# Kernel optimization log

Measured on AMD Instinct MI355X. Metric: run time of the kernel, lower is better.

Reference implementation:

```python
import jax, jax.numpy as jnp
import numpy as np
import math

B, T, C, H, L, V = 4, 2048, 256, 4, 2, 1024
HS = C // H  # head size


def setup_inputs() -> dict:
    key = jax.random.key(0)
    ks = jax.random.split(key, 10)
    s = 0.02
    return {
        "tokens": jax.random.randint(ks[0], (B, T), 0, V),
        "wte": s * jax.random.normal(ks[1], (V + 1, C), dtype=jnp.float32),
        "ln1_g": jnp.ones((L, C), jnp.float32),
        "ln1_b": jnp.zeros((L, C), jnp.float32),
        "attn_w": s * jax.random.normal(ks[2], (L, 3 * C, C), dtype=jnp.float32),
        "attn_b": jnp.zeros((L, 3 * C), jnp.float32),
        "proj_w": s * jax.random.normal(ks[3], (L, C, C), dtype=jnp.float32),
        "proj_b": jnp.zeros((L, C), jnp.float32),
        "embk": s * jax.random.normal(ks[4], (L, T, HS), dtype=jnp.float32),
        "embv": s * jax.random.normal(ks[5], (L, T, HS), dtype=jnp.float32),
        "ln2_g": jnp.ones((L, C), jnp.float32),
        "ln2_b": jnp.zeros((L, C), jnp.float32),
        "fc_w": s * jax.random.normal(ks[6], (L, 4 * C, C), dtype=jnp.float32),
        "fc_b": jnp.zeros((L, 4 * C), jnp.float32),
        "mproj_w": s * jax.random.normal(ks[7], (L, C, 4 * C), dtype=jnp.float32),
        "mproj_b": jnp.zeros((L, C), jnp.float32),
        "lnf_g": jnp.ones((C,), jnp.float32),
        "lnf_b": jnp.zeros((C,), jnp.float32),
        "head_w": s * jax.random.normal(ks[8], (V, C), dtype=jnp.float32),
    }


def _ln(x, g, b):
    mu = x.mean(-1, keepdims=True)
    var = x.var(-1, keepdims=True)
    return (x - mu) / jnp.sqrt(var + 1e-5) * g + b


def _gelu(x):  # NewGELU (tanh approximation)
    return 0.5 * x * (1.0 + jnp.tanh(math.sqrt(2.0 / math.pi) * (x + 0.044715 * x ** 3)))


def reference(tokens, wte, ln1_g, ln1_b, attn_w, attn_b, proj_w, proj_b,
              embk, embv, ln2_g, ln2_b, fc_w, fc_b, mproj_w, mproj_b,
              lnf_g, lnf_b, head_w):
    x = wte[tokens]  # [B,T,C]; no absolute pos emb in this model
    idx = jnp.arange(T)
    rel = jnp.tril(idx[:, None] - idx[None, :])  # [T,T] nonneg offsets
    causal = idx[:, None] >= idx[None, :]
    scale = 1.0 / math.sqrt(HS)
    for l in range(L):
        h = _ln(x, ln1_g[l], ln1_b[l])
        qkv = h @ attn_w[l].T + attn_b[l]  # [B,T,3C]
        q, k, v = jnp.split(qkv, 3, axis=-1)
        q = q.reshape(B, T, H, HS).transpose(0, 2, 1, 3)  # [B,H,T,hs]
        k = k.reshape(B, T, H, HS).transpose(0, 2, 1, 3)
        v = v.reshape(B, T, H, HS).transpose(0, 2, 1, 3)
        rk = embk[l][rel]  # [T,T,hs]
        rv = embv[l][rel]  # [T,T,hs]
        att = jnp.einsum('bhtd,bhsd->bhts', q, k) * scale \
            + jnp.einsum('bhtd,tsd->bhts', q, rk)
        att = jnp.where(causal, att, -jnp.inf)
        att = jax.nn.softmax(att, axis=-1)
        y = jnp.einsum('bhts,bhsd->bhtd', att, v) \
            + jnp.einsum('bhts,tsd->bhtd', att, rv)
        y = y.transpose(0, 2, 1, 3).reshape(B, T, C)
        x = x + (y @ proj_w[l].T + proj_b[l])
        h2 = _ln(x, ln2_g[l], ln2_b[l])
        x = x + (_gelu(h2 @ fc_w[l].T + fc_b[l]) @ mproj_w[l].T + mproj_b[l])
    x = _ln(x, lnf_g, lnf_b)
    return x @ head_w.T  # [B,T,V] logits
```

## Files before the change

### kernel.cpp

```cpp
#include <hip/hip_runtime.h>
#include <hip/hip_bf16.h>
#include <math.h>

#define BB 4
#define TT 2048
#define CC 256
#define HH 4
#define LL 2
#define VV 1024
#define HS 64
#define EPAD 2176
#define LOG2E 1.4426950408889634f

typedef __attribute__((ext_vector_type(8))) __bf16 bf16x8;
typedef __attribute__((ext_vector_type(4))) float f32x4;

#define MFMA16(a, b, c) __builtin_amdgcn_mfma_f32_16x16x32_bf16((a), (b), (c), 0, 0, 0)

__device__ __forceinline__ ushort f2bf(float f) {
    __hip_bfloat16 h = __float2bfloat16(f);
    return *reinterpret_cast<ushort*>(&h);
}
__device__ __forceinline__ float bf2f(ushort u) {
    union { uint i; float f; } c; c.i = ((uint)u) << 16; return c.f;
}

__device__ __forceinline__ void gload16(const void* g, void* l) {
    __builtin_amdgcn_global_load_lds(
        (const __attribute__((address_space(1))) void*)g,
        (__attribute__((address_space(3))) void*)l, 16, 0, 0);
}

__device__ __forceinline__ float gelu_f(float v) {
    return 0.5f * v * (1.0f + tanhf(0.7978845608028654f * (v + 0.044715f * v * v * v)));
}

__global__ void embed_kernel(const int* __restrict__ tok,
                             const float* __restrict__ wte,
                             float* __restrict__ x) {
    int row = blockIdx.x;
    int tid = threadIdx.x;
    int tk = tok[row];
    x[(size_t)row * CC + tid] = wte[(size_t)tk * CC + tid];
}

__global__ void cvt5_kernel(const float* __restrict__ w0, const float* __restrict__ w1,
                            const float* __restrict__ w2, const float* __restrict__ w3,
                            const float* __restrict__ w4,
                            ushort* __restrict__ o0, ushort* __restrict__ o1,
                            ushort* __restrict__ o2, ushort* __restrict__ o3,
                            ushort* __restrict__ o4) {
    int i = blockIdx.x * 256 + threadIdx.x;
    const float* src; ushort* dst; int j;
    if (i < 98304)       { src = w0; dst = o0; j = i; }
    else if (i < 131072) { src = w1; dst = o1; j = i - 98304; }
    else if (i < 262144) { src = w2; dst = o2; j = i - 131072; }
    else if (i < 393216) { src = w3; dst = o3; j = i - 262144; }
    else                 { src = w4; dst = o4; j = i - 393216; }
    float4 v = ((const float4*)src)[j];
    ushort4 o;
    o.x = f2bf(v.x); o.y = f2bf(v.y); o.z = f2bf(v.z); o.w = f2bf(v.w);
    ((ushort4*)dst)[j] = o;
}

__global__ __launch_bounds__(256) void ln_kernel(const float* __restrict__ x,
                                                 const float* __restrict__ g,
                                                 const float* __restrict__ b,
                                                 ushort* __restrict__ out) {
    int row = blockIdx.x * 4 + (threadIdx.x >> 6);
    int lane = threadIdx.x & 63;
    float4 v = ((const float4*)(x + (size_t)row * CC))[lane];
    float s = v.x + v.y + v.z + v.w;
    float s2 = v.x * v.x + v.y * v.y + v.z * v.z + v.w * v.w;
    for (int m = 1; m < 64; m <<= 1) {
        s += __shfl_xor(s, m);
        s2 += __shfl_xor(s2, m);
    }
    float mean = s * (1.0f / CC);
    float var = s2 * (1.0f / CC) - mean * mean;
    float rs = rsqrtf(var + 1e-5f);
    float4 gg = ((const float4*)g)[lane];
    float4 bb = ((const float4*)b)[lane];
    ushort4 o;
    o.x = f2bf((v.x - mean) * rs * gg.x + bb.x);
    o.y = f2bf((v.y - mean) * rs * gg.y + bb.y);
    o.z = f2bf((v.z - mean) * rs * gg.z + bb.z);
    o.w = f2bf((v.w - mean) * rs * gg.w + bb.w);
    ((ushort4*)(out + (size_t)row * CC))[lane] = o;
}

template<int MODE>
__global__ __launch_bounds__(256) void bgemm128_kernel(
        const ushort* __restrict__ A, const ushort* __restrict__ W,
        const float* __restrict__ bias, float* __restrict__ out,
        ushort* __restrict__ outb, int N, int K,
        ushort* __restrict__ qb, ushort* __restrict__ kb,
        ushort* __restrict__ vtb) {
    constexpr int ASUB = 8, TOT = 12, BUFSH = 192 * 32;
    __shared__ ushort lds[2 * BUFSH];
    int tid = threadIdx.x;
    int w = tid >> 6, lane = tid & 63;
    int lo = lane & 15, hi = lane >> 4;
    int row0 = blockIdx.y * 128;
    int col0 = blockIdx.x * 64;
    int wm = w >> 1, wn = w & 1;
    const ushort* Asrc = A + (size_t)row0 * K;
    const ushort* Wsrc = W + (size_t)col0 * K;

    auto STAGE = [&](int buf, int k0) {
        ushort* dst = &lds[buf * BUFSH];
        for (int s = w; s < TOT; s += 4) {
            const ushort* src;
            if (s < ASUB) src = Asrc + (size_t)(s * 16 + lo) * K + k0 + hi * 8;
            else          src = Wsrc + (size_t)((s - ASUB) * 16 + lo) * K + k0 + hi * 8;
            gload16(src, dst + s * 512);
        }
    };

    f32x4 acc[4][2] = {};
    int NT = K >> 5;
    STAGE(0, 0);
    asm volatile("s_waitcnt vmcnt(0)" ::: "memory");
    __syncthreads();
    for (int t = 0; t < NT; ++t) {
        int buf = t & 1;
        if (t + 1 < NT) STAGE(buf ^ 1, (t + 1) << 5);
        bf16x8 a[4], b[2];
#pragma unroll
        for (int f = 0; f < 4; ++f)
            a[f] = *(const bf16x8*)&lds[buf * BUFSH + (wm * 4 + f) * 512 + lane * 8];
#pragma unroll
        for (int g = 0; g < 2; ++g)
            b[g] = *(const bf16x8*)&lds[buf * BUFSH + (ASUB + wn * 2 + g) * 512 + lane * 8];
        __builtin_amdgcn_s_setprio(1);
#pragma unroll
        for (int f = 0; f < 4; ++f)
#pragma unroll
            for (int g = 0; g < 2; ++g)
                acc[f][g] = MFMA16(a[f], b[g], acc[f][g]);
        __builtin_amdgcn_s_setprio(0);
        asm volatile("s_waitcnt vmcnt(0)" ::: "memory");
        __syncthreads();
    }
#pragma unroll
    for (int f = 0; f < 4; ++f) {
        int rr = row0 + wm * 64 + f * 16 + hi * 4;
#pragma unroll
        for (int g = 0; g < 2; ++g) {
            int cc = col0 + wn * 32 + g * 16 + lo;
            float bv = bias ? bias[cc] : 0.0f;
#pragma unroll
            for (int j = 0; j < 4; ++j) {
                int r = rr + j;
                float v = acc[f][g][j] + bv;
                if (MODE == 3) {
                    int t = r & 2047, bb2 = r >> 11;
                    int which = cc >> 8, hh = (cc >> 6) & 3, dd = cc & 63;
                    size_t bh = (size_t)(bb2 * 4 + hh);
                    if (which == 0)      qb[(bh * 2048 + t) * 64 + dd] = f2bf(v);
                    else if (which == 1) kb[(bh * 2048 + t) * 64 + dd] = f2bf(v * (0.125f * LOG2E));
                    else                 vtb[(bh * 64 + dd) * 2048 + t] = f2bf(v);
                } else if (MODE == 2) {
                    outb[(size_t)r * N + cc] = f2bf(gelu_f(v));
                } else {
                    out[(size_t)r * N + cc] = v;
                }
            }
        }
    }
}

__global__ __launch_bounds__(256) void bgemm64_kernel(
        const ushort* __restrict__ A, const ushort* __restrict__ W,
        const float* __restrict__ bias, float* __restrict__ out,
        int N, int K) {
    constexpr int ASUB = 8, TOT = 16, BUFSH = 128 * 64;
    __shared__ ushort lds[2 * BUFSH];
    int tid = threadIdx.x;
    int w = tid >> 6, lane = tid & 63;
    int lo = lane & 15, hi = lane >> 4;
    int row0 = blockIdx.y * 64;
    int col0 = blockIdx.x * 64;
    const ushort* Asrc = A + (size_t)row0 * K;
    const ushort* Wsrc = W + (size_t)col0 * K;

    auto STAGE = [&](int buf, int k0) {
        ushort* dst = &lds[buf * BUFSH];
        for (int s = w; s < TOT; s += 4) {
            const ushort* src;
            if (s < ASUB) {
                int rg = s >> 1, kh = s & 1;
                src = Asrc + (size_t)(rg * 16 + lo) * K + k0 + kh * 32 + hi * 8;
            } else {
                int s2 = s - ASUB;
                int cg = s2 >> 1, kh = s2 & 1;
                src = Wsrc + (size_t)(cg * 16 + lo) * K + k0 + kh * 32 + hi * 8;
            }
            gload16(src, dst + s * 512);
        }
    };

    f32x4 acc[4] = {};
    int NT = K >> 6;
    STAGE(0, 0);
    asm volatile("s_waitcnt vmcnt(0)" ::: "memory");
    __syncthreads();
    for (int t = 0; t < NT; ++t) {
        int buf = t & 1;
        if (t + 1 < NT) STAGE(buf ^ 1, (t + 1) << 6);
        bf16x8 a[2];
#pragma unroll
        for (int kh = 0; kh < 2; ++kh)
            a[kh] = *(const bf16x8*)&lds[buf * BUFSH + (w * 2 + kh) * 512 + lane * 8];
        __builtin_amdgcn_s_setprio(1);
#pragma unroll
        for (int g = 0; g < 4; ++g) {
#pragma unroll
            for (int kh = 0; kh < 2; ++kh) {
                bf16x8 b = *(const bf16x8*)&lds[buf * BUFSH + (ASUB + g * 2 + kh) * 512 + lane * 8];
                acc[g] = MFMA16(a[kh], b, acc[g]);
            }
        }
        __builtin_amdgcn_s_setprio(0);
        asm volatile("s_waitcnt vmcnt(0)" ::: "memory");
        __syncthreads();
    }
#pragma unroll
    for (int g = 0; g < 4; ++g) {
        int cc = col0 + g * 16 + lo;
        float bv = bias ? bias[cc] : 0.0f;
#pragma unroll
        for (int j = 0; j < 4; ++j) {
            int r = row0 + w * 16 + hi * 4 + j;
            out[(size_t)r * N + cc] += acc[g][j] + bv;
        }
    }
}

__global__ void emb_bf_kernel(const float* __restrict__ ek,
                              const float* __restrict__ ev,
                              ushort* __restrict__ ekp,
                              ushort* __restrict__ evtp) {
    int i = blockIdx.x * 256 + threadIdx.x;
    int rp = i >> 6, d = i & 63;
    int o = rp - 64;
    bool in = (o >= 0 && o < TT);
    float kv = in ? ek[(size_t)o * 64 + d] * LOG2E : 0.0f;
    float vv = in ? ev[(size_t)o * 64 + d] : 0.0f;
    ekp[(size_t)rp * 64 + d] = f2bf(kv);
    evtp[(size_t)d * EPAD + rp] = f2bf(vv);
}

#define SBUF 57344
#define KOFF 0
#define VOFF 8192
#define EKOFF 16384
#define EVOFF 32768
#define WSCR (2 * SBUF)

__global__ __launch_bounds__(256, 2) void flash_kernel(
        const ushort* __restrict__ qb,
        const ushort* __restrict__ kb,
        const ushort* __restrict__ vtb,
        const ushort* __restrict__ ekp,
        const ushort* __restrict__ evtp,
        ushort* __restrict__ y) {
    extern __shared__ __align__(16) char dls[];

    int g = blockIdx.x;
    int lbid = ((g & 7) << 5) | (g >> 3);
    int bh = lbid >> 4;
    int pk = lbid & 15;
    int tid = threadIdx.x;
    int sub = tid >> 6;
    int lane = tid & 63;
    int lo = lane & 15, hi = lane >> 4;
    int sw = (lo & 7) << 4;

    char* wbase = dls + WSCR + sub * 7424;
    ushort (*Rl)[88]   = (ushort (*)[88])  wbase;
    ushort (*Pl)[72]   = (ushort (*)[72])  wbase;
    ushort (*Ppl)[104] = (ushort (*)[104])(wbase + 4096);

    {
        uint* pz = reinterpret_cast<uint*>(&Ppl[0][0]);
        for (int i = lane; i < 832; i += 64) pz[i] = 0;
    }

    const char* kB  = (const char*)(kb  + (size_t)bh * 2048 * 64);
    const char* vB  = (const char*)(vtb + (size_t)bh * 64 * 2048);
    const char* ekB = (const char*)ekp;
    const char* evB = (const char*)evtp;

    int t0A = (31 - pk) * 64, t0B = pk * 64;
    int NSA = 32 - pk;
    const int NC = 33;

    auto STAGE = [&](int buf, int ci) {
        int t0 = (ci < NSA) ? t0A : t0B;
        int s0 = ((ci < NSA) ? ci : ci - NSA) * 64;
        int band0 = t0 - s0;
        char* B = dls + buf * SBUF;
#pragma unroll
        for (int p = 0; p < 2; ++p) {
            int gb = p * 4096 + tid * 16;
            int r = gb >> 7, c = gb & 127;
            gload16(kB + (size_t)(s0 + r) * 128 + (c ^ ((r & 7) << 4)),
                    B + KOFF + p * 4096 + ((tid & 192) << 4));
        }
#pragma unroll
        for (int p = 0; p < 2; ++p) {
            int gb = p * 4096 + tid * 16;
            int r = gb >> 7, c = gb & 127;
            gload16(vB + (size_t)r * 4096 + (size_t)s0 * 2 + (c ^ ((r & 7) << 4)),
                    B + VOFF + p * 4096 + ((tid & 192) << 4));
        }
#pragma unroll
        for (int p = 0; p < 4; ++p) {
            int gb = p * 4096 + tid * 16;
            int r = gb >> 7, c = gb & 127;
            gload16(ekB + (size_t)(band0 + r) * 128 + (c ^ ((r & 7) << 4)),
                    B + EKOFF + p * 4096 + ((tid & 192) << 4));
        }
#pragma unroll
        for (int p = 0; p < 6; ++p) {
            int gb = p * 4096 + tid * 16;
            int r = gb / 384, c = gb - r * 384;
            gload16(evB + (size_t)r * 4352 + (size_t)band0 * 2 + (c ^ ((r & 7) << 4)),
                    B + EVOFF + p * 4096 + ((tid & 192) << 4));
        }
    };

    STAGE(0, 0);
    asm volatile("s_waitcnt vmcnt(0)" ::: "memory");
    __syncthreads();

    int b_ = bh >> 2, h_ = bh & 3;
    int buf = 0, ci = 0;

    for (int tile = 0; tile < 2; ++tile) {
        int t0 = tile ? t0B : t0A;
        int NS = tile ? (pk + 1) : NSA;

        const ushort* qbase = qb + ((size_t)bh * 2048 + t0 + sub * 16) * 64;
        bf16x8 qf0 = *(const bf16x8*)(qbase + (size_t)lo * 64 + hi * 8);
        bf16x8 qf1 = *(const bf16x8*)(qbase + (size_t)lo * 64 + 32 + hi * 8);

        float rs[4] = {0.0f, 0.0f, 0.0f, 0.0f};
        f32x4 O[4] = {};

        for (int c = 0; c < NS; ++c, ++ci) {
            if (ci + 1 < NC) STAGE(buf ^ 1, ci + 1);
            const char* B = dls + buf * SBUF;
            bool diag = (c == NS - 1);

            f32x4 sacc[4] = {};
            __builtin_amdgcn_s_setprio(1);
#pragma unroll
            for (int n = 0; n < 4; ++n) {
                int R = n * 16 + lo;
                bf16x8 b0 = *(const bf16x8*)(B + KOFF + R * 128 + ((hi * 16) ^ sw));
                bf16x8 b1 = *(const bf16x8*)(B + KOFF + R * 128 + ((64 + hi * 16) ^ sw));
                sacc[n] = MFMA16(qf0, b0, sacc[n]);
                sacc[n] = MFMA16(qf1, b1, sacc[n]);
            }
#pragma unroll
            for (int n = 0; n < 5; ++n) {
                int RL = (sub + n) * 16 + lo;
                f32x4 r = {};
                bf16x8 e0 = *(const bf16x8*)(B + EKOFF + RL * 128 + ((hi * 16) ^ sw));
                bf16x8 e1 = *(const bf16x8*)(B + EKOFF + RL * 128 + ((64 + hi * 16) ^ sw));
                r = MFMA16(qf0, e0, r);
                r = MFMA16(qf1, e1, r);
#pragma unroll
                for (int j = 0; j < 4; ++j) Rl[hi * 4 + j][n * 16 + lo] = f2bf(r[j]);
            }
            __builtin_amdgcn_s_setprio(0);
            float sv[4][4];
#pragma unroll
            for (int n = 0; n < 4; ++n) {
                int sl = n * 16 + lo;
#pragma unroll
                for (int j = 0; j < 4; ++j) {
                    int r_ = hi * 4 + j;
                    sv[n][j] = sacc[n][j] + bf2f(Rl[r_][r_ - sl + 64]);
                }
            }
            asm volatile("" ::: "memory");
#pragma unroll
            for (int n = 0; n < 4; ++n) {
                int sl = n * 16 + lo;
#pragma unroll
                for (int j = 0; j < 4; ++j) {
                    int r_ = hi * 4 + j;
                    float p;
                    if (diag) p = (sl <= sub * 16 + r_) ? exp2f(sv[n][j]) : 0.0f;
                    else      p = exp2f(sv[n][j]);
                    rs[j] += p;
                    ushort pu = f2bf(p);
                    Pl[r_][sl] = pu;
                    Ppl[r_][r_ - sl + 64] = pu;
                }
            }

            __builtin_amdgcn_s_setprio(1);
#pragma unroll
            for (int n = 0; n < 4; ++n) {
                int R = n * 16 + lo;
#pragma unroll
                for (int kc = 0; kc < 2; ++kc) {
                    bf16x8 a = *(const bf16x8*)(&Pl[lo][kc * 32 + hi * 8]);
                    bf16x8 b = *(const bf16x8*)(B + VOFF + R * 128 + ((kc * 64 + hi * 16) ^ sw));
                    O[n] = MFMA16(a, b, O[n]);
                }
#pragma unroll
                for (int kc = 0; kc < 3; ++kc) {
                    bf16x8 a = *(const bf16x8*)(&Ppl[lo][kc * 32 + hi * 8]);
                    bf16x8 b = *(const bf16x8*)(B + EVOFF + R * 384 +
                                                ((sub * 32 + kc * 64 + hi * 16) ^ sw));
                    O[n] = MFMA16(a, b, O[n]);
                }
            }
            __builtin_amdgcn_s_setprio(0);
            asm volatile("" ::: "memory");

            asm volatile("s_waitcnt vmcnt(0)" ::: "memory");
            __syncthreads();
            buf ^= 1;
        }

#pragma unroll
        for (int msk = 1; msk < 16; msk <<= 1)
#pragma unroll
            for (int j = 0; j < 4; ++j) rs[j] += __shfl_xor(rs[j], msk);
        float inv[4];
#pragma unroll
        for (int j = 0; j < 4; ++j) inv[j] = 1.0f / rs[j];
#pragma unroll
        for (int n = 0; n < 4; ++n)
#pragma unroll
            for (int j = 0; j < 4; ++j) {
                int r = t0 + sub * 16 + hi * 4 + j;
                y[((size_t)(b_ * 2048 + r)) * 256 + h_ * 64 + n * 16 + lo] =
                    f2bf(O[n][j] * inv[j]);
            }
    }
}

extern "C" void kernel_launch(void* const* d_in, const int* in_sizes, int n_in,
                              void* d_out, int out_size, void* d_ws, size_t ws_size,
                              hipStream_t stream) {
    const int*   tokens  = (const int*)d_in[0];
    const float* wte     = (const float*)d_in[1];
    const float* ln1_g   = (const float*)d_in[2];
    const float* ln1_b   = (const float*)d_in[3];
    const float* attn_w  = (const float*)d_in[4];
    const float* attn_b  = (const float*)d_in[5];
    const float* proj_w  = (const float*)d_in[6];
    const float* proj_b  = (const float*)d_in[7];
    const float* embk    = (const float*)d_in[8];
    const float* embv    = (const float*)d_in[9];
    const float* ln2_g   = (const float*)d_in[10];
    const float* ln2_b   = (const float*)d_in[11];
    const float* fc_w    = (const float*)d_in[12];
    const float* fc_b    = (const float*)d_in[13];
    const float* mproj_w = (const float*)d_in[14];
    const float* mproj_b = (const float*)d_in[15];
    const float* lnf_g   = (const float*)d_in[16];
    const float* lnf_b   = (const float*)d_in[17];
    const float* head_w  = (const float*)d_in[18];
    float* out = (float*)d_out;

    const int M = BB * TT;
    char* wsb = (char*)d_ws;
    float*  x    = (float*)wsb;
    ushort* h    = (ushort*)(wsb + ((size_t)8 << 20));
    ushort* y    = (ushort*)(wsb + ((size_t)12 << 20));
    ushort* qb   = (ushort*)(wsb + ((size_t)16 << 20));
    ushort* kbf  = (ushort*)(wsb + ((size_t)20 << 20));
    ushort* vtb  = (ushort*)(wsb + ((size_t)24 << 20));
    ushort* ekp  = (ushort*)(wsb + ((size_t)28 << 20));
    ushort* evtp = (ushort*)(wsb + ((size_t)28 << 20) + 524288);
    ushort* attn_wb  = (ushort*)(wsb + ((size_t)29 << 20));
    ushort* proj_wb  = attn_wb + (size_t)LL * 3 * CC * CC;
    ushort* fc_wb    = proj_wb + (size_t)LL * CC * CC;
    ushort* mproj_wb = fc_wb + (size_t)LL * 4 * CC * CC;
    ushort* head_wb  = mproj_wb + (size_t)LL * CC * 4 * CC;
    ushort* fcb = (ushort*)d_out;

    dim3 blk(256);
    const int FLDS = WSCR + 4 * 7424;
    hipFuncSetAttribute(reinterpret_cast<const void*>(flash_kernel),
                        hipFuncAttributeMaxDynamicSharedMemorySize, FLDS);

    cvt5_kernel<<<dim3(1792), blk, 0, stream>>>(
        attn_w, proj_w, fc_w, mproj_w, head_w,
        attn_wb, proj_wb, fc_wb, mproj_wb, head_wb);

    embed_kernel<<<dim3(M), blk, 0, stream>>>(tokens, wte, x);

    for (int l = 0; l < LL; l++) {
        ln_kernel<<<dim3(M / 4), blk, 0, stream>>>(x, ln1_g + l * CC, ln1_b + l * CC, h);
        bgemm128_kernel<3><<<dim3(12, 64), blk, 0, stream>>>(
            h, attn_wb + (size_t)l * 3 * CC * CC, attn_b + (size_t)l * 3 * CC,
            nullptr, nullptr, 3 * CC, CC, qb, kbf, vtb);
        emb_bf_kernel<<<dim3(EPAD * 64 / 256), blk, 0, stream>>>(
            embk + (size_t)l * TT * HS, embv + (size_t)l * TT * HS, ekp, evtp);
        flash_kernel<<<dim3(256), blk, FLDS, stream>>>(qb, kbf, vtb, ekp, evtp, y);
        bgemm64_kernel<<<dim3(4, 128), blk, 0, stream>>>(
            y, proj_wb + (size_t)l * CC * CC, proj_b + (size_t)l * CC,
            x, CC, CC);
        ln_kernel<<<dim3(M / 4), blk, 0, stream>>>(x, ln2_g + l * CC, ln2_b + l * CC, h);
        bgemm128_kernel<2><<<dim3(16, 64), blk, 0, stream>>>(
            h, fc_wb + (size_t)l * 4 * CC * CC, fc_b + (size_t)l * 4 * CC,
            nullptr, fcb, 4 * CC, CC, nullptr, nullptr, nullptr);
        bgemm64_kernel<<<dim3(4, 128), blk, 0, stream>>>(
            fcb, mproj_wb + (size_t)l * CC * 4 * CC, mproj_b + (size_t)l * CC,
            x, CC, 4 * CC);
    }

    ln_kernel<<<dim3(M / 4), blk, 0, stream>>>(x, lnf_g, lnf_b, h);
    bgemm128_kernel<0><<<dim3(16, 64), blk, 0, stream>>>(
        h, head_wb, nullptr, out, nullptr, VV, CC, nullptr, nullptr, nullptr);
}
```

Baseline: 350.6 us.

## Split flash attention work across 8 waves with LDS reduction of partial outputs

Doubles the flash attention block to 512 threads, pairing waves so each computes half of the key columns for scores and half of the P·V/P·Ev contraction for the same query rows. Partial output accumulators and row sums are combined through LDS scratch at the end of each query tile. This aims to raise wave-level parallelism and latency hiding per CU, at the cost of extra barriers, an LDS reduction step, and a tighter LDS footprint.

```diff
diff --git a/kernel.cpp b/kernel.cpp
--- a/kernel.cpp
+++ b/kernel.cpp
@@ -258,7 +258,7 @@
 #define EVOFF 32768
 #define WSCR (2 * SBUF)
 
-__global__ __launch_bounds__(256, 2) void flash_kernel(
+__global__ __launch_bounds__(512, 2) void flash_kernel(
         const ushort* __restrict__ qb,
         const ushort* __restrict__ kb,
         const ushort* __restrict__ vtb,
@@ -272,15 +272,17 @@
     int bh = lbid >> 4;
     int pk = lbid & 15;
     int tid = threadIdx.x;
-    int sub = tid >> 6;
+    int w = tid >> 6;
+    int sub = w & 3;
+    int h = w >> 2;
     int lane = tid & 63;
     int lo = lane & 15, hi = lane >> 4;
     int sw = (lo & 7) << 4;
 
-    char* wbase = dls + WSCR + sub * 7424;
+    char* wbase = dls + WSCR + w * 6144;
     ushort (*Rl)[88]   = (ushort (*)[88])  wbase;
     ushort (*Pl)[72]   = (ushort (*)[72])  wbase;
-    ushort (*Ppl)[104] = (ushort (*)[104])(wbase + 4096);
+    ushort (*Ppl)[104] = (ushort (*)[104])(wbase + 2816);
 
     {
         uint* pz = reinterpret_cast<uint*>(&Ppl[0][0]);
@@ -301,33 +303,31 @@
         int s0 = ((ci < NSA) ? ci : ci - NSA) * 64;
         int band0 = t0 - s0;
         char* B = dls + buf * SBUF;
-#pragma unroll
-        for (int p = 0; p < 2; ++p) {
-            int gb = p * 4096 + tid * 16;
+        int wb = (tid & 448) << 4;
+        {
+            int gb = tid * 16;
             int r = gb >> 7, c = gb & 127;
-            gload16(kB + (size_t)(s0 + r) * 128 + (c ^ ((r & 7) << 4)),
-                    B + KOFF + p * 4096 + ((tid & 192) << 4));
-        }
-#pragma unroll
-        for (int p = 0; p < 2; ++p) {
-            int gb = p * 4096 + tid * 16;
+            gload16(kB + (size_t)(s0 + r) * 128 + (c ^ ((r & 7) << 4)), B + KOFF + wb);
+        }
+        {
+            int gb = tid * 16;
             int r = gb >> 7, c = gb & 127;
             gload16(vB + (size_t)r * 4096 + (size_t)s0 * 2 + (c ^ ((r & 7) << 4)),
-                    B + VOFF + p * 4096 + ((tid & 192) << 4));
-        }
-#pragma unroll
-        for (int p = 0; p < 4; ++p) {
-            int gb = p * 4096 + tid * 16;
+                    B + VOFF + wb);
+        }
+#pragma unroll
+        for (int p = 0; p < 2; ++p) {
+            int gb = p * 8192 + tid * 16;
             int r = gb >> 7, c = gb & 127;
             gload16(ekB + (size_t)(band0 + r) * 128 + (c ^ ((r & 7) << 4)),
-                    B + EKOFF + p * 4096 + ((tid & 192) << 4));
-        }
-#pragma unroll
-        for (int p = 0; p < 6; ++p) {
-            int gb = p * 4096 + tid * 16;
+                    B + EKOFF + p * 8192 + wb);
+        }
+#pragma unroll
+        for (int p = 0; p < 3; ++p) {
+            int gb = p * 8192 + tid * 16;
             int r = gb / 384, c = gb - r * 384;
             gload16(evB + (size_t)r * 4352 + (size_t)band0 * 2 + (c ^ ((r & 7) << 4)),
-                    B + EVOFF + p * 4096 + ((tid & 192) << 4));
+                    B + EVOFF + p * 8192 + wb);
         }
     };
 
@@ -337,6 +337,8 @@
 
     int b_ = bh >> 2, h_ = bh & 3;
     int buf = 0, ci = 0;
+    int nb = h ? 0 : 2;
+    int kcA = h ? 0 : 1, kcB = h ? 1 : 2;
 
     for (int tile = 0; tile < 2; ++tile) {
         int t0 = tile ? t0B : t0A;
@@ -354,18 +356,19 @@
             const char* B = dls + buf * SBUF;
             bool diag = (c == NS - 1);
 
-            f32x4 sacc[4] = {};
+            f32x4 sacc[2] = {};
             __builtin_amdgcn_s_setprio(1);
 #pragma unroll
-            for (int n = 0; n < 4; ++n) {
-                int R = n * 16 + lo;
+            for (int ni = 0; ni < 2; ++ni) {
+                int R = (2 * h + ni) * 16 + lo;
                 bf16x8 b0 = *(const bf16x8*)(B + KOFF + R * 128 + ((hi * 16) ^ sw));
                 bf16x8 b1 = *(const bf16x8*)(B + KOFF + R * 128 + ((64 + hi * 16) ^ sw));
-                sacc[n] = MFMA16(qf0, b0, sacc[n]);
-                sacc[n] = MFMA16(qf1, b1, sacc[n]);
-            }
-#pragma unroll
-            for (int n = 0; n < 5; ++n) {
+                sacc[ni] = MFMA16(qf0, b0, sacc[ni]);
+                sacc[ni] = MFMA16(qf1, b1, sacc[ni]);
+            }
+#pragma unroll
+            for (int ni = 0; ni < 3; ++ni) {
+                int n = nb + ni;
                 int RL = (sub + n) * 16 + lo;
                 f32x4 r = {};
                 bf16x8 e0 = *(const bf16x8*)(B + EKOFF + RL * 128 + ((hi * 16) ^ sw));
@@ -376,50 +379,47 @@
                 for (int j = 0; j < 4; ++j) Rl[hi * 4 + j][n * 16 + lo] = f2bf(r[j]);
             }
             __builtin_amdgcn_s_setprio(0);
-            float sv[4][4];
-#pragma unroll
-            for (int n = 0; n < 4; ++n) {
-                int sl = n * 16 + lo;
+            float sv[2][4];
+#pragma unroll
+            for (int ni = 0; ni < 2; ++ni) {
+                int sl = (2 * h + ni) * 16 + lo;
 #pragma unroll
                 for (int j = 0; j < 4; ++j) {
                     int r_ = hi * 4 + j;
-                    sv[n][j] = sacc[n][j] + bf2f(Rl[r_][r_ - sl + 64]);
+                    sv[ni][j] = sacc[ni][j] + bf2f(Rl[r_][r_ - sl + 64]);
                 }
             }
             asm volatile("" ::: "memory");
 #pragma unroll
-            for (int n = 0; n < 4; ++n) {
-                int sl = n * 16 + lo;
+            for (int ni = 0; ni < 2; ++ni) {
+                int sl = (2 * h + ni) * 16 + lo;
 #pragma unroll
                 for (int j = 0; j < 4; ++j) {
                     int r_ = hi * 4 + j;
-                    float p;
-                    if (diag) p = (sl <= sub * 16 + r_) ? exp2f(sv[n][j]) : 0.0f;
-                    else      p = exp2f(sv[n][j]);
+                    float p = (!diag || sl <= sub * 16 + r_) ? exp2f(sv[ni][j]) : 0.0f;
                     rs[j] += p;
                     ushort pu = f2bf(p);
                     Pl[r_][sl] = pu;
                     Ppl[r_][r_ - sl + 64] = pu;
                 }
             }
+            asm volatile("" ::: "memory");
 
             __builtin_amdgcn_s_setprio(1);
+            bf16x8 pa  = *(const bf16x8*)(&Pl[lo][h * 32 + hi * 8]);
+            bf16x8 pb0 = *(const bf16x8*)(&Ppl[lo][kcA * 32 + hi * 8]);
+            bf16x8 pb1 = *(const bf16x8*)(&Ppl[lo][kcB * 32 + hi * 8]);
 #pragma unroll
             for (int n = 0; n < 4; ++n) {
                 int R = n * 16 + lo;
-#pragma unroll
-                for (int kc = 0; kc < 2; ++kc) {
-                    bf16x8 a = *(const bf16x8*)(&Pl[lo][kc * 32 + hi * 8]);
-                    bf16x8 b = *(const bf16x8*)(B + VOFF + R * 128 + ((kc * 64 + hi * 16) ^ sw));
-                    O[n] = MFMA16(a, b, O[n]);
-                }
-#pragma unroll
-                for (int kc = 0; kc < 3; ++kc) {
-                    bf16x8 a = *(const bf16x8*)(&Ppl[lo][kc * 32 + hi * 8]);
-                    bf16x8 b = *(const bf16x8*)(B + EVOFF + R * 384 +
-                                                ((sub * 32 + kc * 64 + hi * 16) ^ sw));
-                    O[n] = MFMA16(a, b, O[n]);
-                }
+                bf16x8 bv = *(const bf16x8*)(B + VOFF + R * 128 + ((h * 64 + hi * 16) ^ sw));
+                O[n] = MFMA16(pa, bv, O[n]);
+                bf16x8 e0 = *(const bf16x8*)(B + EVOFF + R * 384 +
+                                             ((sub * 32 + kcA * 64 + hi * 16) ^ sw));
+                O[n] = MFMA16(pb0, e0, O[n]);
+                bf16x8 e1 = *(const bf16x8*)(B + EVOFF + R * 384 +
+                                             ((sub * 32 + kcB * 64 + hi * 16) ^ sw));
+                O[n] = MFMA16(pb1, e1, O[n]);
             }
             __builtin_amdgcn_s_setprio(0);
             asm volatile("" ::: "memory");
@@ -433,17 +433,38 @@
         for (int msk = 1; msk < 16; msk <<= 1)
 #pragma unroll
             for (int j = 0; j < 4; ++j) rs[j] += __shfl_xor(rs[j], msk);
-        float inv[4];
-#pragma unroll
-        for (int j = 0; j < 4; ++j) inv[j] = 1.0f / rs[j];
-#pragma unroll
-        for (int n = 0; n < 4; ++n)
-#pragma unroll
-            for (int j = 0; j < 4; ++j) {
-                int r = t0 + sub * 16 + hi * 4 + j;
-                y[((size_t)(b_ * 2048 + r)) * 256 + h_ * 64 + n * 16 + lo] =
-                    f2bf(O[n][j] * inv[j]);
-            }
+
+        char* mscr = dls + (buf ^ 1) * SBUF + sub * 8192;
+        if (h == 1) {
+            float* Of = (float*)mscr;
+#pragma unroll
+            for (int n = 0; n < 4; ++n)
+#pragma unroll
+                for (int j = 0; j < 4; ++j)
+                    Of[(hi * 4 + j) * 64 + n * 16 + lo] = O[n][j];
+            if (lo == 0)
+#pragma unroll
+                for (int j = 0; j < 4; ++j)
+                    ((float*)(mscr + 4096))[hi * 4 + j] = rs[j];
+        }
+        __syncthreads();
+        if (h == 0) {
+            float* Of = (float*)mscr;
+            float inv[4];
+#pragma unroll
+            for (int j = 0; j < 4; ++j)
+                inv[j] = 1.0f / (rs[j] + ((float*)(mscr + 4096))[hi * 4 + j]);
+#pragma unroll
+            for (int n = 0; n < 4; ++n)
+#pragma unroll
+                for (int j = 0; j < 4; ++j) {
+                    int r = t0 + sub * 16 + hi * 4 + j;
+                    float v = O[n][j] + Of[(hi * 4 + j) * 64 + n * 16 + lo];
+                    y[((size_t)(b_ * 2048 + r)) * 256 + h_ * 64 + n * 16 + lo] =
+                        f2bf(v * inv[j]);
+                }
+        }
+        __syncthreads();
     }
 }
 
@@ -489,7 +510,7 @@
     ushort* fcb = (ushort*)d_out;
 
     dim3 blk(256);
-    const int FLDS = WSCR + 4 * 7424;
+    const int FLDS = WSCR + 8 * 6144;
     hipFuncSetAttribute(reinterpret_cast<const void*>(flash_kernel),
                         hipFuncAttributeMaxDynamicSharedMemorySize, FLDS);
 
@@ -506,7 +527,7 @@
             nullptr, nullptr, 3 * CC, CC, qb, kbf, vtb);
         emb_bf_kernel<<<dim3(EPAD * 64 / 256), blk, 0, stream>>>(
             embk + (size_t)l * TT * HS, embv + (size_t)l * TT * HS, ekp, evtp);
-        flash_kernel<<<dim3(256), blk, FLDS, stream>>>(qb, kbf, vtb, ekp, evtp, y);
+        flash_kernel<<<dim3(256), dim3(512), FLDS, stream>>>(qb, kbf, vtb, ekp, evtp, y);
         bgemm64_kernel<<<dim3(4, 128), blk, 0, stream>>>(
             y, proj_wb + (size_t)l * CC * CC, proj_b + (size_t)l * CC,
             x, CC, CC);
```

Result: faster. 335.5 us (-4.3%).
